# Performance work log

Measured on AMD Instinct MI355X. Metric: run time of the kernel, lower is better.

## Reference

```python
import jax, jax.numpy as jnp
import numpy as np

B, D, NSEQ = 8, 512, 32
L0 = NSEQ * NSEQ          # 1024
H, DH = 8, 64             # n_head, d_head; H*DH == D
DFF = 2048
NLAYER = 2
EPS = 1e-6
SCALE = 1.0 / (DH ** 0.5)


def setup_inputs() -> dict:
    key = jax.random.key(0)
    ks = jax.random.split(key, 16)
    s = lambda fan: 1.0 / np.sqrt(fan)
    return {
        "embed1": jax.random.normal(ks[0], (B, D, L0), jnp.float32),
        "embed2": jax.random.normal(ks[1], (B, D, L0), jnp.float32),
        "cls_token": jax.random.normal(ks[2], (1, 1, D), jnp.float32),
        "Wq": jax.random.normal(ks[3], (NLAYER, D, D), jnp.float32) * s(D),
        "bq": jnp.zeros((NLAYER, D), jnp.float32),
        "Wk": jax.random.normal(ks[4], (NLAYER, D, D), jnp.float32) * s(D),
        "bk": jnp.zeros((NLAYER, D), jnp.float32),
        "Wv": jax.random.normal(ks[5], (NLAYER, D, D), jnp.float32) * s(D),
        "bv": jnp.zeros((NLAYER, D), jnp.float32),
        "Wo": jax.random.normal(ks[6], (NLAYER, D, D), jnp.float32) * s(D),
        "bo": jnp.zeros((NLAYER, D), jnp.float32),
        "ln1_g": jnp.ones((NLAYER, D), jnp.float32),
        "ln1_b": jnp.zeros((NLAYER, D), jnp.float32),
        "W1": jax.random.normal(ks[7], (NLAYER, DFF, D), jnp.float32) * s(D),
        "b1": jnp.zeros((NLAYER, DFF), jnp.float32),
        "W2": jax.random.normal(ks[8], (NLAYER, D, DFF), jnp.float32) * s(DFF),
        "b2": jnp.zeros((NLAYER, D), jnp.float32),
        "ln2_g": jnp.ones((NLAYER, D), jnp.float32),
        "ln2_b": jnp.zeros((NLAYER, D), jnp.float32),
    }


def _ln(x, g, b):
    m = jnp.mean(x, axis=-1, keepdims=True)
    v = jnp.mean(jnp.square(x - m), axis=-1, keepdims=True)
    return (x - m) * jax.lax.rsqrt(v + EPS) * g + b


def reference(embed1, embed2, cls_token, Wq, bq, Wk, bk, Wv, bv, Wo, bo,
              ln1_g, ln1_b, W1, b1, W2, b2, ln2_g, ln2_b):
    b = embed1.shape[0]
    cls = jnp.broadcast_to(cls_token, (b, 1, D))
    # [B, L0, D] with prepended cls -> [B, L, D]
    x1 = jnp.concatenate([cls, jnp.transpose(embed1, (0, 2, 1))], axis=1)
    x2 = jnp.concatenate([cls, jnp.transpose(embed2, (0, 2, 1))], axis=1)
    # mask_inputs is all ones vs i_pad=0 -> attn_mask all False (no masking)
    x = x1
    for l in range(NLAYER):
        q = (x  @ Wq[l].T + bq[l]).reshape(b, -1, H, DH)   # [B,L,H,DH]
        k = (x2 @ Wk[l].T + bk[l]).reshape(b, -1, H, DH)
        v = (x2 @ Wv[l].T + bv[l]).reshape(b, -1, H, DH)
        scores = jnp.einsum('bqhd,bkhd->bhqk', q, k) * SCALE
        attn = jax.nn.softmax(scores, axis=-1)
        ctx = jnp.einsum('bhqk,bkhd->bqhd', attn, v).reshape(b, -1, H * DH)
        att_out = ctx @ Wo[l].T + bo[l]
        x = _ln(x + att_out, ln1_g[l], ln1_b[l])
        h = jax.nn.gelu(x @ W1[l].T + b1[l], approximate=False)
        ffn = h @ W2[l].T + b2[l]
        x = _ln(x + ffn, ln2_g[l], ln2_b[l])
    return x
```

## Files before the change

### kernel.cpp

```cpp
#include <hip/hip_runtime.h>
#include <hip/hip_bf16.h>

constexpr int B_   = 8;
constexpr int D_   = 512;
constexpr int L0_  = 1024;
constexpr int L_   = 1025;
constexpr int H_   = 8;
constexpr int DH_  = 64;
constexpr int DFF_ = 2048;
constexpr int NLAYER_ = 2;
constexpr int M_   = B_ * L_;
constexpr int LP_  = 1088;
constexpr int NQT_ = 9;
constexpr int NSPLIT_ = 4;
constexpr float EPS_   = 1e-6f;
constexpr float QSCALE_ = 0.18033688011112042f;

#define DEV_INLINE __device__ __forceinline__

typedef __attribute__((ext_vector_type(8)))  __bf16 bf16x8;
typedef __attribute__((ext_vector_type(4)))  __bf16 bf16x4;
typedef __attribute__((ext_vector_type(4)))  float  f32x4;
typedef __attribute__((ext_vector_type(16))) float  f32x16;
typedef __attribute__((ext_vector_type(4)))  unsigned int u32x4;
typedef __attribute__((ext_vector_type(2)))  unsigned int u32x2;

union U4 { uint32_t u[4]; bf16x8 f; };

DEV_INLINE float gelu_exact(float x) {
    return 0.5f * x * (1.f + erff(x * 0.70710678118654752f));
}

DEV_INLINE uint16_t bfbits(float v) {
    __bf16 h = (__bf16)v;
    return __builtin_bit_cast(uint16_t, h);
}
DEV_INLINE uint32_t pk2f(float a, float b) {
    return (uint32_t)bfbits(a) | ((uint32_t)bfbits(b) << 16);
}
DEV_INLINE float bf2f(uint32_t bits16) {
    uint32_t u = bits16 << 16;
    return __builtin_bit_cast(float, u);
}
DEV_INLINE uint32_t b32f(float f) { return __builtin_bit_cast(uint32_t, f); }
DEV_INLINE float f32b(uint32_t u) { return __builtin_bit_cast(float, u); }

DEV_INLINE void gload16(const __bf16* g, __bf16* l) {
    __builtin_amdgcn_global_load_lds(
        (const __attribute__((address_space(1))) void*)g,
        (__attribute__((address_space(3))) void*)l,
        16, 0, 0);
}

__global__ __launch_bounds__(256) void tobf16_kernel(
    const float* __restrict__ src, __bf16* __restrict__ dst, int n4) {
    int i = blockIdx.x * 256 + threadIdx.x;
    if (i >= n4) return;
    float4 v = *(const float4*)&src[i * 4];
    bf16x4 h;
    h[0] = (__bf16)v.x; h[1] = (__bf16)v.y;
    h[2] = (__bf16)v.z; h[3] = (__bf16)v.w;
    *(bf16x4*)&dst[i * 4] = h;
}

__global__ __launch_bounds__(256) void zero_vt_pad_kernel(__bf16* __restrict__ Vt) {
    constexpr int PAD = LP_ - L_;
    int idx = blockIdx.x * 256 + threadIdx.x;
    int total = B_ * H_ * DH_ * PAD;
    if (idx >= total) return;
    int row = idx / PAD;
    int c   = idx - row * PAD;
    Vt[(size_t)row * LP_ + L_ + c] = (__bf16)0.f;
}

__global__ __launch_bounds__(256) void write_cls_kernel(
    const float* __restrict__ cls, float* __restrict__ X1, float* __restrict__ X2) {
    int idx = blockIdx.x * 256 + threadIdx.x;
    int b = idx >> 9;
    int d = idx & 511;
    float v = cls[d];
    X1[(size_t)b * L_ * D_ + d] = v;
    X2[(size_t)b * L_ * D_ + d] = v;
}

__global__ __launch_bounds__(256) void transpose_embed_kernel(
    const float* __restrict__ e, float* __restrict__ X) {
    __shared__ float tile[32][33];
    int b  = blockIdx.z;
    int i0 = blockIdx.x * 32;
    int d0 = blockIdx.y * 32;
    int tx = threadIdx.x;
    int ty = threadIdx.y;
#pragma unroll
    for (int j = 0; j < 32; j += 8)
        tile[ty + j][tx] = e[((size_t)b * D_ + d0 + ty + j) * L0_ + i0 + tx];
    __syncthreads();
#pragma unroll
    for (int j = 0; j < 32; j += 8)
        X[((size_t)b * L_ + 1 + i0 + ty + j) * D_ + d0 + tx] = tile[tx][ty + j];
}

template <bool GELU, int OUTMODE>
__global__ __launch_bounds__(256) void gemm_mfma_kernel(
    const __bf16* __restrict__ A, const __bf16* __restrict__ Wh,
    const float* __restrict__ bias, float* __restrict__ C,
    __bf16* __restrict__ Ch, int M, int N, int K, float oscale) {
    constexpr int BM = 128, BN = 64, BK = 64;
    __shared__ alignas(16) __bf16 Ahs[BM * BK];
    __shared__ alignas(16) __bf16 Bhs[BN * BK];

    const int GN = N / BN;
    const int nwg = gridDim.x;
    int bid = blockIdx.x;
    {
        int q = nwg >> 3, r = nwg & 7;
        int xcd = bid & 7, pos = bid >> 3;
        bid = (xcd < r) ? xcd * (q + 1) + pos
                        : r * (q + 1) + (xcd - r) * q + pos;
    }
    const int bm = bid / GN;
    const int bn = bid % GN;
    const int m0 = bm * BM;
    const int n0 = bn * BN;

    const int tid  = threadIdx.x;
    const int lane = tid & 63;
    const int wv   = tid >> 6;
    const int wr   = wv >> 1;
    const int wc   = wv & 1;
    const int fr   = lane & 15;
    const int fq   = lane >> 4;
    const int fq8  = fq * 8;
    const int mb   = wr * 64;
    const int nb   = wc * 32;
    const int swz  = (fr & 7) << 3;

    const int srcColE = (((lane & 7) ^ (lane >> 3)) << 3);
    size_t aSrc[4];
#pragma unroll
    for (int j = 0; j < 4; ++j) {
        int row = (wv * 4 + j) * 8 + (lane >> 3);
        int ar = m0 + row; if (ar > M - 1) ar = M - 1;
        aSrc[j] = (size_t)ar * K + srcColE;
    }
    size_t bSrc[2];
#pragma unroll
    for (int j = 0; j < 2; ++j) {
        int row = (wv * 2 + j) * 8 + (lane >> 3);
        bSrc[j] = (size_t)(n0 + row) * K + srcColE;
    }

    f32x4 acc[4][2];
#pragma unroll
    for (int i = 0; i < 4; ++i)
#pragma unroll
        for (int j = 0; j < 2; ++j) acc[i][j] = (f32x4){0.f, 0.f, 0.f, 0.f};

    const int nk = K / BK;
#pragma unroll
    for (int j = 0; j < 4; ++j) gload16(A + aSrc[j], &Ahs[(wv * 4 + j) * 512]);
#pragma unroll
    for (int j = 0; j < 2; ++j) gload16(Wh + bSrc[j], &Bhs[(wv * 2 + j) * 512]);

    for (int kt = 0; kt < nk; ++kt) {
        __syncthreads();

#pragma unroll
        for (int ks = 0; ks < 2; ++ks) {
            bf16x8 ah[4], bh[2];
#pragma unroll
            for (int i = 0; i < 4; ++i)
                ah[i] = *(bf16x8*)&Ahs[(mb + i * 16 + fr) * 64 + ((ks * 32 + fq8) ^ swz)];
#pragma unroll
            for (int j = 0; j < 2; ++j)
                bh[j] = *(bf16x8*)&Bhs[(nb + j * 16 + fr) * 64 + ((ks * 32 + fq8) ^ swz)];
#pragma unroll
            for (int i = 0; i < 4; ++i)
#pragma unroll
                for (int j = 0; j < 2; ++j)
                    acc[i][j] = __builtin_amdgcn_mfma_f32_16x16x32_bf16(ah[i], bh[j], acc[i][j], 0, 0, 0);
        }
        __syncthreads();

        if (kt + 1 < nk) {
            int k0 = (kt + 1) * BK;
#pragma unroll
            for (int j = 0; j < 4; ++j) gload16(A + aSrc[j] + k0, &Ahs[(wv * 4 + j) * 512]);
#pragma unroll
            for (int j = 0; j < 2; ++j) gload16(Wh + bSrc[j] + k0, &Bhs[(wv * 2 + j) * 512]);
        }
    }

    const int ccol0 = n0 + nb + fr;
    const float b0 = bias[ccol0];
    const float b1 = bias[ccol0 + 16];
#pragma unroll
    for (int i = 0; i < 4; ++i) {
#pragma unroll
        for (int r = 0; r < 4; ++r) {
            int row = m0 + mb + i * 16 + fq * 4 + r;
            if (row < M) {
                float v0 = acc[i][0][r] + b0;
                float v1 = acc[i][1][r] + b1;
                if (GELU) { v0 = gelu_exact(v0); v1 = gelu_exact(v1); }
                v0 *= oscale;
                v1 *= oscale;
                if (OUTMODE == 2) {
                    Ch[(size_t)row * N + ccol0]      = (__bf16)v0;
                    Ch[(size_t)row * N + ccol0 + 16] = (__bf16)v1;
                } else {
                    C[(size_t)row * N + ccol0]      = v0;
                    C[(size_t)row * N + ccol0 + 16] = v1;
                }
            }
        }
    }
}

__global__ __launch_bounds__(256) void gemm_kv_kernel(
    const __bf16* __restrict__ A, const __bf16* __restrict__ Wh,
    const float* __restrict__ biasK, const float* __restrict__ biasV,
    __bf16* __restrict__ Kb, __bf16* __restrict__ Vt) {
    constexpr int BM = 128, BN = 64, BK = 64, K = 512, N = 1024;
    __shared__ alignas(16) __bf16 Ahs[BM * BK];
    __shared__ alignas(16) __bf16 Bhs[BN * BK];

    constexpr int GN = N / BN;
    const int nwg = gridDim.x;
    int bid = blockIdx.x;
    {
        int q = nwg >> 3, r = nwg & 7;
        int xcd = bid & 7, pos = bid >> 3;
        bid = (xcd < r) ? xcd * (q + 1) + pos
                        : r * (q + 1) + (xcd - r) * q + pos;
    }
    const int bm = bid / GN;
    const int bn = bid % GN;
    const int m0 = bm * BM;
    const int n0 = bn * BN;

    const int tid  = threadIdx.x;
    const int lane = tid & 63;
    const int wv   = tid >> 6;
    const int wr   = wv >> 1;
    const int wc   = wv & 1;
    const int fr   = lane & 15;
    const int fq   = lane >> 4;
    const int fq8  = fq * 8;
    const int mb   = wr * 64;
    const int nb   = wc * 32;
    const int swz  = (fr & 7) << 3;

    const int srcColE = (((lane & 7) ^ (lane >> 3)) << 3);
    size_t aSrc[4];
#pragma unroll
    for (int j = 0; j < 4; ++j) {
        int row = (wv * 4 + j) * 8 + (lane >> 3);
        int ar = m0 + row; if (ar > M_ - 1) ar = M_ - 1;
        aSrc[j] = (size_t)ar * K + srcColE;
    }
    size_t bSrc[2];
#pragma unroll
    for (int j = 0; j < 2; ++j) {
        int row = (wv * 2 + j) * 8 + (lane >> 3);
        bSrc[j] = (size_t)(n0 + row) * K + srcColE;
    }

    f32x4 acc[4][2];
#pragma unroll
    for (int i = 0; i < 4; ++i)
#pragma unroll
        for (int j = 0; j < 2; ++j) acc[i][j] = (f32x4){0.f, 0.f, 0.f, 0.f};

    const int nk = K / BK;
#pragma unroll
    for (int j = 0; j < 4; ++j) gload16(A + aSrc[j], &Ahs[(wv * 4 + j) * 512]);
#pragma unroll
    for (int j = 0; j < 2; ++j) gload16(Wh + bSrc[j], &Bhs[(wv * 2 + j) * 512]);

    for (int kt = 0; kt < nk; ++kt) {
        __syncthreads();

#pragma unroll
        for (int ks = 0; ks < 2; ++ks) {
            bf16x8 ah[4], bh[2];
#pragma unroll
            for (int i = 0; i < 4; ++i)
                ah[i] = *(bf16x8*)&Ahs[(mb + i * 16 + fr) * 64 + ((ks * 32 + fq8) ^ swz)];
#pragma unroll
            for (int j = 0; j < 2; ++j)
                bh[j] = *(bf16x8*)&Bhs[(nb + j * 16 + fr) * 64 + ((ks * 32 + fq8) ^ swz)];
#pragma unroll
            for (int i = 0; i < 4; ++i)
#pragma unroll
                for (int j = 0; j < 2; ++j)
                    acc[i][j] = __builtin_amdgcn_mfma_f32_16x16x32_bf16(ah[i], bh[j], acc[i][j], 0, 0, 0);
        }
        __syncthreads();

        if (kt + 1 < nk) {
            int k0 = (kt + 1) * BK;
#pragma unroll
            for (int j = 0; j < 4; ++j) gload16(A + aSrc[j] + k0, &Ahs[(wv * 4 + j) * 512]);
#pragma unroll
            for (int j = 0; j < 2; ++j) gload16(Wh + bSrc[j] + k0, &Bhs[(wv * 2 + j) * 512]);
        }
    }

    const int ccol0 = n0 + nb + fr;
    if (n0 < 512) {
        const float b0 = biasK[ccol0];
        const float b1 = biasK[ccol0 + 16];
#pragma unroll
        for (int i = 0; i < 4; ++i) {
#pragma unroll
            for (int r = 0; r < 4; ++r) {
                int row = m0 + mb + i * 16 + fq * 4 + r;
                if (row < M_) {
                    Kb[(size_t)row * 512 + ccol0]      = (__bf16)(acc[i][0][r] + b0);
                    Kb[(size_t)row * 512 + ccol0 + 16] = (__bf16)(acc[i][1][r] + b1);
                }
            }
        }
    } else {
        const int cv = ccol0 - 512;
        const int h2 = cv >> 6, d2 = cv & 63;
        const float b0 = biasV[cv];
        const float b1 = biasV[cv + 16];
#pragma unroll
        for (int i = 0; i < 4; ++i) {
#pragma unroll
            for (int r = 0; r < 4; ++r) {
                int row = m0 + mb + i * 16 + fq * 4 + r;
                if (row < M_) {
                    int b2 = row / L_;
                    int l2 = row - b2 * L_;
                    size_t vb = (size_t)(b2 * H_ + h2) * DH_ * LP_;
                    Vt[vb + (size_t)d2 * LP_ + l2]        = (__bf16)(acc[i][0][r] + b0);
                    Vt[vb + (size_t)(d2 + 16) * LP_ + l2] = (__bf16)(acc[i][1][r] + b1);
                }
            }
        }
    }
}

__global__ __launch_bounds__(256) void attn_mfma_kernel(
    const __bf16* __restrict__ Qb, const __bf16* __restrict__ Kb,
    const __bf16* __restrict__ Vtb, __bf16* __restrict__ Opart,
    float* __restrict__ ml) {
    constexpr int LDP = 72;
    constexpr int NT = (L_ + 63) / 64;
    __shared__ alignas(16) __bf16 Kls[64][LDP];
    __shared__ alignas(16) __bf16 Vls[64][LDP];

    const int tid  = threadIdx.x;
    const int lane = tid & 63;
    const int wv   = tid >> 6;
    const int la   = lane & 31;
    const int hl   = lane >> 5;

    int bid = blockIdx.x;
    int swz = (bid & 7) * (NSPLIT_ * NQT_ * H_ * B_ / 8) + (bid >> 3);
    const int s   = swz / (NQT_ * H_ * B_);
    int rem = swz - s * (NQT_ * H_ * B_);
    const int qt = rem % NQT_;
    const int bh = rem / NQT_;
    const int h = bh & 7, b = bh >> 3;
    const int q0 = qt * 128 + wv * 32;
    const int T0 = (NT * s) / NSPLIT_;
    const int T1 = (NT * (s + 1)) / NSPLIT_;
    const size_t obase = (size_t)b * L_ * D_ + h * DH_;

    bf16x8 bq[4];
    {
        int gq = q0 + la; if (gq > L_ - 1) gq = L_ - 1;
        const __bf16* qrow = Qb + (size_t)(b * L_ + gq) * D_ + h * DH_;
#pragma unroll
        for (int c = 0; c < 4; ++c)
            bq[c] = *(const bf16x8*)&qrow[c * 16 + hl * 8];
    }

    float m = -1e30f, lsum = 0.f;
    f32x16 oT0, oT1;
#pragma unroll
    for (int r = 0; r < 16; ++r) { oT0[r] = 0.f; oT1[r] = 0.f; }

    const int sr  = tid >> 2;
    const int scb = (tid & 3) * 8;
    const size_t kRowBase = (size_t)(b * L_) * D_ + h * DH_ + scb;
    const size_t vRowBase = ((size_t)bh * DH_ + sr) * LP_ + scb;

    u32x4 kR[2], vR[2];
    {
        int gr = T0 * 64 + sr; if (gr > L_ - 1) gr = L_ - 1;
        const __bf16* kp = Kb + kRowBase + (size_t)gr * D_;
        const __bf16* vp = Vtb + vRowBase + T0 * 64;
        kR[0] = *(const u32x4*)&kp[0];  kR[1] = *(const u32x4*)&kp[32];
        vR[0] = *(const u32x4*)&vp[0];  vR[1] = *(const u32x4*)&vp[32];
        *(u32x4*)&Kls[sr][scb]      = kR[0];
        *(u32x4*)&Kls[sr][scb + 32] = kR[1];
        *(u32x4*)&Vls[sr][scb]      = vR[0];
        *(u32x4*)&Vls[sr][scb + 32] = vR[1];
    }

    for (int t = T0; t < T1; ++t) {
        const int kt = t * 64;
        __syncthreads();

        if (t + 1 < T1) {
            int gr = kt + 64 + sr; if (gr > L_ - 1) gr = L_ - 1;
            const __bf16* kp = Kb + kRowBase + (size_t)gr * D_;
            const __bf16* vp = Vtb + vRowBase + (kt + 64);
            kR[0] = *(const u32x4*)&kp[0];  kR[1] = *(const u32x4*)&kp[32];
            vR[0] = *(const u32x4*)&vp[0];  vR[1] = *(const u32x4*)&vp[32];
        }

        const bool fullTile = (kt + 64 <= L_);
#pragma unroll
        for (int st = 0; st < 2; ++st) {
            const int ko = st * 32;

            f32x16 sacc;
#pragma unroll
            for (int r = 0; r < 16; ++r) sacc[r] = 0.f;
            __builtin_amdgcn_s_setprio(1);
#pragma unroll
            for (int c = 0; c < 4; ++c) {
                bf16x8 ak = *(bf16x8*)&Kls[ko + la][c * 16 + hl * 8];
                sacc = __builtin_amdgcn_mfma_f32_32x32x16_bf16(ak, bq[c], sacc, 0, 0, 0);
            }
            __builtin_amdgcn_s_setprio(0);

            float p[16];
            if (fullTile) {
#pragma unroll
                for (int r = 0; r < 16; ++r) p[r] = sacc[r];
            } else {
#pragma unroll
                for (int r = 0; r < 16; ++r) {
                    int kg = kt + ko + (r & 3) + 8 * (r >> 2) + 4 * hl;
                    p[r] = (kg < L_) ? sacc[r] : -1e30f;
                }
            }

            float q0m = fmaxf(fmaxf(p[0], p[1]),  fmaxf(p[2], p[3]));
            float q1m = fmaxf(fmaxf(p[4], p[5]),  fmaxf(p[6], p[7]));
            float q2m = fmaxf(fmaxf(p[8], p[9]),  fmaxf(p[10], p[11]));
            float q3m = fmaxf(fmaxf(p[12], p[13]), fmaxf(p[14], p[15]));
            float t0 = fmaxf(fmaxf(q0m, q1m), fmaxf(q2m, q3m));
            u32x2 rm = __builtin_amdgcn_permlane32_swap(b32f(t0), b32f(t0), false, false);
            t0 = fmaxf(f32b(rm[0]), f32b(rm[1]));
            float mn = fmaxf(m, t0);
            const bool noresc = __all(mn == m);
            float sclq = noresc ? 1.f : __builtin_amdgcn_exp2f(m - mn);
            m = mn;
#pragma unroll
            for (int r = 0; r < 16; ++r) p[r] = __builtin_amdgcn_exp2f(p[r] - mn);
            float s0 = (p[0] + p[1]) + (p[2] + p[3]);
            float s1 = (p[4] + p[5]) + (p[6] + p[7]);
            float s2 = (p[8] + p[9]) + (p[10] + p[11]);
            float s3 = (p[12] + p[13]) + (p[14] + p[15]);
            float ls = (s0 + s1) + (s2 + s3);
            u32x2 rl = __builtin_amdgcn_permlane32_swap(b32f(ls), b32f(ls), false, false);
            ls = f32b(rl[0]) + f32b(rl[1]);
            lsum = lsum * sclq + ls;
            if (!noresc) {
#pragma unroll
                for (int r = 0; r < 16; ++r) { oT0[r] *= sclq; oT1[r] *= sclq; }
            }

            bf16x8 pb[2];
#pragma unroll
            for (int cc = 0; cc < 2; ++cc) {
                uint32_t G0 = pk2f(p[8 * cc + 0], p[8 * cc + 1]);
                uint32_t G1 = pk2f(p[8 * cc + 2], p[8 * cc + 3]);
                uint32_t G2 = pk2f(p[8 * cc + 4], p[8 * cc + 5]);
                uint32_t G3 = pk2f(p[8 * cc + 6], p[8 * cc + 7]);
                u32x2 r02 = __builtin_amdgcn_permlane32_swap(G0, G2, false, false);
                u32x2 r13 = __builtin_amdgcn_permlane32_swap(G1, G3, false, false);
                U4 uh;
                uh.u[0] = r02[0]; uh.u[1] = r13[0];
                uh.u[2] = r02[1]; uh.u[3] = r13[1];
                pb[cc] = uh.f;
            }

            __builtin_amdgcn_s_setprio(1);
#pragma unroll
            for (int cc = 0; cc < 2; ++cc) {
                bf16x8 av0 = *(bf16x8*)&Vls[la][ko + cc * 16 + hl * 8];
                bf16x8 av1 = *(bf16x8*)&Vls[32 + la][ko + cc * 16 + hl * 8];
                oT0 = __builtin_amdgcn_mfma_f32_32x32x16_bf16(av0, pb[cc], oT0, 0, 0, 0);
                oT1 = __builtin_amdgcn_mfma_f32_32x32x16_bf16(av1, pb[cc], oT1, 0, 0, 0);
            }
            __builtin_amdgcn_s_setprio(0);
        }

        __syncthreads();
        if (t + 1 < T1) {
            *(u32x4*)&Kls[sr][scb]      = kR[0];
            *(u32x4*)&Kls[sr][scb + 32] = kR[1];
            *(u32x4*)&Vls[sr][scb]      = vR[0];
            *(u32x4*)&Vls[sr][scb + 32] = vR[1];
        }
    }

    __bf16* Op = Opart + (size_t)s * M_ * D_;
    int qrow = q0 + la;
    if (qrow < L_) {
        __bf16* orow = Op + obase + (size_t)qrow * D_;
#pragma unroll
        for (int bb = 0; bb < 4; ++bb) {
            uint2 uu0, uu1;
            uu0.x = pk2f(oT0[4 * bb + 0], oT0[4 * bb + 1]);
            uu0.y = pk2f(oT0[4 * bb + 2], oT0[4 * bb + 3]);
            uu1.x = pk2f(oT1[4 * bb + 0], oT1[4 * bb + 1]);
            uu1.y = pk2f(oT1[4 * bb + 2], oT1[4 * bb + 3]);
            *(uint2*)&orow[bb * 8 + hl * 4]      = uu0;
            *(uint2*)&orow[32 + bb * 8 + hl * 4] = uu1;
        }
        if (hl == 0) {
            size_t mlidx = (((size_t)s * B_ + b) * H_ + h) * L_ + qrow;
            ml[mlidx * 2]     = m;
            ml[mlidx * 2 + 1] = lsum;
        }
    }
}

__global__ __launch_bounds__(256) void attn_merge_kernel(
    const __bf16* __restrict__ Opart, const float* __restrict__ ml,
    __bf16* __restrict__ Out) {
    int idx = blockIdx.x * 256 + threadIdx.x;
    if (idx >= M_ * 64) return;
    int row = idx >> 6;
    int seg = idx & 63;
    int col0 = seg * 8;
    int h = col0 >> 6;
    int b = row / L_;
    int l = row - b * L_;
    float ms[NSPLIT_], ls[NSPLIT_];
    float mm = -1e30f;
#pragma unroll
    for (int s = 0; s < NSPLIT_; ++s) {
        size_t mi = ((((size_t)s * B_ + b) * H_ + h) * L_ + l) * 2;
        ms[s] = ml[mi];
        ls[s] = ml[mi + 1];
        mm = fmaxf(mm, ms[s]);
    }
    float wsum = 0.f, w[NSPLIT_];
#pragma unroll
    for (int s = 0; s < NSPLIT_; ++s) {
        w[s] = __builtin_amdgcn_exp2f(ms[s] - mm);
        wsum += w[s] * ls[s];
    }
    float inv = 1.f / wsum;
#pragma unroll
    for (int s = 0; s < NSPLIT_; ++s) w[s] *= inv;

    size_t base = (size_t)row * D_ + col0;
    float o[8] = {0.f, 0.f, 0.f, 0.f, 0.f, 0.f, 0.f, 0.f};
#pragma unroll
    for (int s = 0; s < NSPLIT_; ++s) {
        const __bf16* Os = Opart + (size_t)s * M_ * D_;
        u32x4 a = *(const u32x4*)&Os[base];
#pragma unroll
        for (int i = 0; i < 4; ++i) {
            o[2 * i]     += w[s] * bf2f(a[i] & 0xffffu);
            o[2 * i + 1] += w[s] * bf2f(a[i] >> 16);
        }
    }
    U4 u;
#pragma unroll
    for (int i = 0; i < 4; ++i)
        u.u[i] = pk2f(o[2 * i], o[2 * i + 1]);
    *(u32x4*)&Out[base] = *(u32x4*)&u.u[0];
}

template <bool HIOUT>
__global__ __launch_bounds__(256) void add_ln_kernel(
    const float* __restrict__ X, const __bf16* __restrict__ Y,
    const float* __restrict__ g, const float* __restrict__ be,
    float* __restrict__ Out, __bf16* __restrict__ Oh) {
    int wave = threadIdx.x >> 6;
    int lane = threadIdx.x & 63;
    int row = blockIdx.x * 4 + wave;
    if (row >= M_) return;
    size_t base = (size_t)row * D_;
    int c0 = lane * 4, c1 = 256 + lane * 4;
    float4 xa = *(const float4*)&X[base + c0];
    float4 xb = *(const float4*)&X[base + c1];
    u32x2 ya = *(const u32x2*)&Y[base + c0];
    u32x2 yb = *(const u32x2*)&Y[base + c1];
    float v[8] = {xa.x + bf2f(ya[0] & 0xffffu), xa.y + bf2f(ya[0] >> 16),
                  xa.z + bf2f(ya[1] & 0xffffu), xa.w + bf2f(ya[1] >> 16),
                  xb.x + bf2f(yb[0] & 0xffffu), xb.y + bf2f(yb[0] >> 16),
                  xb.z + bf2f(yb[1] & 0xffffu), xb.w + bf2f(yb[1] >> 16)};
    float s = 0.f, s2 = 0.f;
#pragma unroll
    for (int i = 0; i < 8; ++i) { s += v[i]; s2 = fmaf(v[i], v[i], s2); }
#pragma unroll
    for (int off = 32; off > 0; off >>= 1) {
        s  += __shfl_xor(s, off);
        s2 += __shfl_xor(s2, off);
    }
    float mean = s * (1.f / D_);
    float var  = s2 * (1.f / D_) - mean * mean;
    float rstd = rsqrtf(var + EPS_);
    float4 ga = *(const float4*)&g[c0];
    float4 gb = *(const float4*)&g[c1];
    float4 ba = *(const float4*)&be[c0];
    float4 bb = *(const float4*)&be[c1];
    float o[8];
    o[0] = (v[0] - mean) * rstd * ga.x + ba.x;
    o[1] = (v[1] - mean) * rstd * ga.y + ba.y;
    o[2] = (v[2] - mean) * rstd * ga.z + ba.z;
    o[3] = (v[3] - mean) * rstd * ga.w + ba.w;
    o[4] = (v[4] - mean) * rstd * gb.x + bb.x;
    o[5] = (v[5] - mean) * rstd * gb.y + bb.y;
    o[6] = (v[6] - mean) * rstd * gb.z + bb.z;
    o[7] = (v[7] - mean) * rstd * gb.w + bb.w;
    *(float4*)&Out[base + c0] = make_float4(o[0], o[1], o[2], o[3]);
    *(float4*)&Out[base + c1] = make_float4(o[4], o[5], o[6], o[7]);
    if (HIOUT) {
        bf16x4 h0, h1;
#pragma unroll
        for (int i = 0; i < 4; ++i) {
            h0[i] = (__bf16)o[i];
            h1[i] = (__bf16)o[4 + i];
        }
        *(bf16x4*)&Oh[base + c0] = h0;
        *(bf16x4*)&Oh[base + c1] = h1;
    }
}

extern "C" void kernel_launch(void* const* d_in, const int* in_sizes, int n_in,
                              void* d_out, int out_size, void* d_ws, size_t ws_size,
                              hipStream_t stream) {
    const float* embed1 = (const float*)d_in[0];
    const float* embed2 = (const float*)d_in[1];
    const float* cls    = (const float*)d_in[2];
    const float* Wq = (const float*)d_in[3];
    const float* bq = (const float*)d_in[4];
    const float* Wk = (const float*)d_in[5];
    const float* bk = (const float*)d_in[6];
    const float* Wv = (const float*)d_in[7];
    const float* bv = (const float*)d_in[8];
    const float* Wo = (const float*)d_in[9];
    const float* bo = (const float*)d_in[10];
    const float* ln1g = (const float*)d_in[11];
    const float* ln1b = (const float*)d_in[12];
    const float* W1 = (const float*)d_in[13];
    const float* b1 = (const float*)d_in[14];
    const float* W2 = (const float*)d_in[15];
    const float* b2 = (const float*)d_in[16];
    const float* ln2g = (const float*)d_in[17];
    const float* ln2b = (const float*)d_in[18];

    const size_t SZ = (size_t)M_ * D_;
    float* ws = (float*)d_ws;
    float* X   = ws;
    __bf16* Xh = (__bf16*)(ws + SZ);
    __bf16* X2h = (__bf16*)(ws + SZ + SZ / 2);
    float* Tb  = ws + 2 * SZ;
    __bf16* Tb2h = (__bf16*)(ws + 2 * SZ);
    __bf16* Tbh = (__bf16*)(ws + 2 * SZ + SZ / 2);
    __bf16* Qbh = (__bf16*)(ws + 3 * SZ);
    __bf16* WoOutH = (__bf16*)(ws + 3 * SZ);
    __bf16* Kbh = (__bf16*)(ws + 4 * SZ);
    __bf16* Vtb = (__bf16*)(ws + 5 * SZ);
    __bf16* Hbh = (__bf16*)(ws + 5 * SZ);
    float* mlBuf   = ws + 6 * SZ + SZ / 2;
    __bf16* Opart  = (__bf16*)(ws + 7 * SZ);
    __bf16* wreg = (__bf16*)(ws + 9 * SZ);

    const size_t NQl = (size_t)D_ * D_;
    const size_t NQ  = (size_t)NLAYER_ * NQl;
    const size_t NF  = (size_t)NLAYER_ * DFF_ * D_;
    __bf16* Wqh  = wreg;
    __bf16* Wkvh = Wqh + NQ;
    __bf16* Woh  = Wkvh + 2 * NQ;
    __bf16* W1h  = Woh + NQ;
    __bf16* W2h  = W1h + NF;

    tobf16_kernel<<<(int)(NQ / 4 + 255) / 256, 256, 0, stream>>>(Wq, Wqh, (int)(NQ / 4));
    tobf16_kernel<<<(int)(NQ / 4 + 255) / 256, 256, 0, stream>>>(Wo, Woh, (int)(NQ / 4));
    tobf16_kernel<<<(int)(NF / 4 + 255) / 256, 256, 0, stream>>>(W1, W1h, (int)(NF / 4));
    tobf16_kernel<<<(int)(NF / 4 + 255) / 256, 256, 0, stream>>>(W2, W2h, (int)(NF / 4));
    for (int l = 0; l < NLAYER_; ++l) {
        tobf16_kernel<<<(int)(NQl / 4 + 255) / 256, 256, 0, stream>>>(
            Wk + l * NQl, Wkvh + l * 2 * NQl, (int)(NQl / 4));
        tobf16_kernel<<<(int)(NQl / 4 + 255) / 256, 256, 0, stream>>>(
            Wv + l * NQl, Wkvh + l * 2 * NQl + NQl, (int)(NQl / 4));
    }

    float* X2tmp = Tb;
    write_cls_kernel<<<(B_ * D_) / 256, 256, 0, stream>>>(cls, X, X2tmp);
    transpose_embed_kernel<<<dim3(L0_ / 32, D_ / 32, B_), dim3(32, 8), 0, stream>>>(embed1, X);
    transpose_embed_kernel<<<dim3(L0_ / 32, D_ / 32, B_), dim3(32, 8), 0, stream>>>(embed2, X2tmp);
    tobf16_kernel<<<(int)(SZ / 4 + 255) / 256, 256, 0, stream>>>(X, Xh, (int)(SZ / 4));
    tobf16_kernel<<<(int)(SZ / 4 + 255) / 256, 256, 0, stream>>>(X2tmp, X2h, (int)(SZ / 4));

    const int GM = (M_ + 127) / 128;
    const int g512  = GM * (512 / 64);
    const int g1024 = GM * (1024 / 64);
    const int g2048 = GM * (2048 / 64);
    const int gpad  = (B_ * H_ * DH_ * (LP_ - L_) + 255) / 256;
    const int gmerge = (M_ * 64 + 255) / 256;

    for (int l = 0; l < NLAYER_; ++l) {
        const size_t oQ = (size_t)l * NQl;
        const size_t oF = (size_t)l * DFF_ * D_;

        gemm_mfma_kernel<false, 2><<<g512, 256, 0, stream>>>(
            Xh, Wqh + oQ, bq + l * D_, nullptr, Qbh, M_, D_, D_, QSCALE_);
        gemm_kv_kernel<<<g1024, 256, 0, stream>>>(
            X2h, Wkvh + l * 2 * NQl, bk + l * D_, bv + l * D_, Kbh, Vtb);
        zero_vt_pad_kernel<<<gpad, 256, 0, stream>>>(Vtb);

        attn_mfma_kernel<<<NSPLIT_ * NQT_ * H_ * B_, 256, 0, stream>>>(
            Qbh, Kbh, Vtb, Opart, mlBuf);
        attn_merge_kernel<<<gmerge, 256, 0, stream>>>(Opart, mlBuf, Tbh);

        gemm_mfma_kernel<false, 2><<<g512, 256, 0, stream>>>(
            Tbh, Woh + oQ, bo + l * D_, nullptr, WoOutH, M_, D_, D_, 1.f);

        add_ln_kernel<true><<<(M_ + 3) / 4, 256, 0, stream>>>(
            X, WoOutH, ln1g + l * D_, ln1b + l * D_, X, Xh);

        gemm_mfma_kernel<true, 2><<<g2048, 256, 0, stream>>>(
            Xh, W1h + oF, b1 + l * DFF_, nullptr, Hbh, M_, DFF_, D_, 1.f);
        gemm_mfma_kernel<false, 2><<<g512, 256, 0, stream>>>(
            Hbh, W2h + oF, b2 + l * D_, nullptr, Tb2h, M_, D_, DFF_, 1.f);

        if (l == NLAYER_ - 1) {
            add_ln_kernel<false><<<(M_ + 3) / 4, 256, 0, stream>>>(
                X, Tb2h, ln2g + l * D_, ln2b + l * D_, (float*)d_out, nullptr);
        } else {
            add_ln_kernel<true><<<(M_ + 3) / 4, 256, 0, stream>>>(
                X, Tb2h, ln2g + l * D_, ln2b + l * D_, X, Xh);
        }
    }
}
```

Measured before the change: 458.7 us.

## Load attention K/V fragments directly from global memory and halve KV split

```diff
diff --git a/kernel.cpp b/kernel.cpp
--- a/kernel.cpp
+++ b/kernel.cpp
@@ -12,7 +12,7 @@
 constexpr int M_   = B_ * L_;
 constexpr int LP_  = 1088;
 constexpr int NQT_ = 9;
-constexpr int NSPLIT_ = 4;
+constexpr int NSPLIT_ = 2;
 constexpr float EPS_   = 1e-6f;
 constexpr float QSCALE_ = 0.18033688011112042f;
 
@@ -348,10 +348,7 @@
     const __bf16* __restrict__ Qb, const __bf16* __restrict__ Kb,
     const __bf16* __restrict__ Vtb, __bf16* __restrict__ Opart,
     float* __restrict__ ml) {
-    constexpr int LDP = 72;
     constexpr int NT = (L_ + 63) / 64;
-    __shared__ alignas(16) __bf16 Kls[64][LDP];
-    __shared__ alignas(16) __bf16 Vls[64][LDP];
 
     const int tid  = threadIdx.x;
     const int lane = tid & 63;
@@ -385,40 +382,19 @@
 #pragma unroll
     for (int r = 0; r < 16; ++r) { oT0[r] = 0.f; oT1[r] = 0.f; }
 
-    const int sr  = tid >> 2;
-    const int scb = (tid & 3) * 8;
-    const size_t kRowBase = (size_t)(b * L_) * D_ + h * DH_ + scb;
-    const size_t vRowBase = ((size_t)bh * DH_ + sr) * LP_ + scb;
-
-    u32x4 kR[2], vR[2];
-    {
-        int gr = T0 * 64 + sr; if (gr > L_ - 1) gr = L_ - 1;
-        const __bf16* kp = Kb + kRowBase + (size_t)gr * D_;
-        const __bf16* vp = Vtb + vRowBase + T0 * 64;
-        kR[0] = *(const u32x4*)&kp[0];  kR[1] = *(const u32x4*)&kp[32];
-        vR[0] = *(const u32x4*)&vp[0];  vR[1] = *(const u32x4*)&vp[32];
-        *(u32x4*)&Kls[sr][scb]      = kR[0];
-        *(u32x4*)&Kls[sr][scb + 32] = kR[1];
-        *(u32x4*)&Vls[sr][scb]      = vR[0];
-        *(u32x4*)&Vls[sr][scb + 32] = vR[1];
-    }
+    const __bf16* kBase = Kb + (size_t)(b * L_) * D_ + h * DH_ + hl * 8;
+    const __bf16* vRow0 = Vtb + ((size_t)bh * DH_ + la) * LP_ + hl * 8;
+    const __bf16* vRow1 = Vtb + ((size_t)bh * DH_ + 32 + la) * LP_ + hl * 8;
 
     for (int t = T0; t < T1; ++t) {
         const int kt = t * 64;
-        __syncthreads();
-
-        if (t + 1 < T1) {
-            int gr = kt + 64 + sr; if (gr > L_ - 1) gr = L_ - 1;
-            const __bf16* kp = Kb + kRowBase + (size_t)gr * D_;
-            const __bf16* vp = Vtb + vRowBase + (kt + 64);
-            kR[0] = *(const u32x4*)&kp[0];  kR[1] = *(const u32x4*)&kp[32];
-            vR[0] = *(const u32x4*)&vp[0];  vR[1] = *(const u32x4*)&vp[32];
-        }
-
         const bool fullTile = (kt + 64 <= L_);
 #pragma unroll
         for (int st = 0; st < 2; ++st) {
             const int ko = st * 32;
+            int krow = kt + ko + la;
+            if (krow > L_ - 1) krow = L_ - 1;
+            const __bf16* kRow = kBase + (size_t)krow * D_;
 
             f32x16 sacc;
 #pragma unroll
@@ -426,7 +402,7 @@
             __builtin_amdgcn_s_setprio(1);
 #pragma unroll
             for (int c = 0; c < 4; ++c) {
-                bf16x8 ak = *(bf16x8*)&Kls[ko + la][c * 16 + hl * 8];
+                bf16x8 ak = *(const bf16x8*)&kRow[c * 16];
                 sacc = __builtin_amdgcn_mfma_f32_32x32x16_bf16(ak, bq[c], sacc, 0, 0, 0);
             }
             __builtin_amdgcn_s_setprio(0);
@@ -487,20 +463,12 @@
             __builtin_amdgcn_s_setprio(1);
 #pragma unroll
             for (int cc = 0; cc < 2; ++cc) {
-                bf16x8 av0 = *(bf16x8*)&Vls[la][ko + cc * 16 + hl * 8];
-                bf16x8 av1 = *(bf16x8*)&Vls[32 + la][ko + cc * 16 + hl * 8];
+                bf16x8 av0 = *(const bf16x8*)&vRow0[kt + ko + cc * 16];
+                bf16x8 av1 = *(const bf16x8*)&vRow1[kt + ko + cc * 16];
                 oT0 = __builtin_amdgcn_mfma_f32_32x32x16_bf16(av0, pb[cc], oT0, 0, 0, 0);
                 oT1 = __builtin_amdgcn_mfma_f32_32x32x16_bf16(av1, pb[cc], oT1, 0, 0, 0);
             }
             __builtin_amdgcn_s_setprio(0);
-        }
-
-        __syncthreads();
-        if (t + 1 < T1) {
-            *(u32x4*)&Kls[sr][scb]      = kR[0];
-            *(u32x4*)&Kls[sr][scb + 32] = kR[1];
-            *(u32x4*)&Vls[sr][scb]      = vR[0];
-            *(u32x4*)&Vls[sr][scb + 32] = vR[1];
         }
     }
 
```

Result: slower. 536.9 us (+17.0%).
